# Kernel tuning notes

Hardware: AMD Instinct MI355X
Metric: run time of the kernel (lower is better)

Reference implementation:

```python
import jax, jax.numpy as jnp
import numpy as np

IGNORE_INDEX = -100
W_HARD = 0.5
W_SOFT = 0.5
TEMPERATURE = 1.0
BETA = 0.0  # forward KL branch
NORMALIZE_TOPK = True


def setup_inputs() -> dict:
    key = jax.random.key(0)
    ks = jax.random.split(key, 6)
    B, N, D, V, K = 2, 2048, 2048, 32768, 64
    student_input = jax.random.normal(ks[0], (B, N, D), dtype=jnp.float32)
    # scale weight so logits are O(1)-ish and logsumexp is well-behaved in fp32
    student_lm_head_weight = jax.random.normal(ks[1], (V, D), dtype=jnp.float32) * 0.02
    target_token_ids = jax.random.randint(ks[2], (B, N, K), 0, V, dtype=jnp.int64)
    # realistic teacher top-k logprobs: normalized over k
    target_logprobs = jax.nn.log_softmax(jax.random.normal(ks[3], (B, N, K), dtype=jnp.float32), axis=-1)
    target_mask = jax.random.randint(ks[4], (B, N, K), 0, 2, dtype=jnp.int32)
    true_labels = jax.random.randint(ks[5], (B, N), 0, V, dtype=jnp.int64)
    return {
        "student_input": student_input,
        "student_lm_head_weight": student_lm_head_weight,
        "target_token_ids": target_token_ids,
        "target_logprobs": target_logprobs,
        "target_mask": target_mask,
        "true_labels": true_labels,
    }


def reference(student_input, student_lm_head_weight, target_token_ids, target_logprobs, target_mask, true_labels):
    B, N, D = student_input.shape
    K = target_token_ids.shape[-1]
    M = B * N

    x = student_input.reshape(M, D)
    logits = x @ student_lm_head_weight.T  # (M, V)

    # ---- hard CE loss on next-token-shifted labels (sum reduction, ignore_index) ----
    labels = jnp.pad(true_labels, ((0, 0), (0, 1)), constant_values=IGNORE_INDEX)[:, 1:].reshape(M)
    lse_full = jax.nn.logsumexp(logits, axis=-1)  # (M,)
    valid = labels != IGNORE_INDEX
    safe_labels = jnp.where(valid, labels, 0)
    gold = jnp.take_along_axis(logits, safe_labels[:, None], axis=-1)[:, 0]
    ce_loss = jnp.sum(jnp.where(valid, lse_full - gold, 0.0))

    # ---- soft top-k forward-KL loss (beta == 0.0) ----
    s_logits = logits / TEMPERATURE
    s_lse = jax.nn.logsumexp(s_logits, axis=-1, keepdims=True)  # (M, 1)
    tk_ids = target_token_ids.reshape(M, K)
    s_lp_topk = jnp.take_along_axis(s_logits, tk_ids, axis=-1) - s_lse  # (M, K)
    if NORMALIZE_TOPK:
        s_lp_topk = jax.nn.log_softmax(s_lp_topk, axis=-1)
    t_lp = target_logprobs.reshape(M, K)
    mask = target_mask.reshape(M, K).astype(bool)
    fwd_kl = jnp.exp(t_lp) * (t_lp - s_lp_topk)  # per-token forward KL terms
    kd_loss = jnp.sum(jnp.where(mask, fwd_kl, 0.0))
    kd_loss = kd_loss * (TEMPERATURE ** 2)

    return W_SOFT * kd_loss + W_HARD * ce_loss
```

## Files before the change

### kernel.cpp

```cpp
#include <hip/hip_runtime.h>
#include <hip/hip_bf16.h>
#include <stdint.h>

typedef __attribute__((ext_vector_type(4))) float f32x4;
typedef __attribute__((ext_vector_type(2))) long l8x16;

#define D_DIM 2048
#define V_DIM 32768
#define M_DIM 4096
#define N_SEQ 2048
#define K_TOP 64
#define NSLOT 512
#define EBCAP 512
#define WSCALE 64.0f
#define IWSCALE 0.015625f

static __device__ __forceinline__ unsigned int f32_to_e4m3(float x) {
  float ax = fminf(fabsf(x), 448.0f);
  unsigned int s = (__float_as_uint(x) >> 31) << 7;
  if (ax >= 0.015625f) {
    unsigned int m = __float_as_uint(ax);
    unsigned int keep = m >> 20;
    unsigned int rb = (m >> 19) & 1u, st = (m & 0x7FFFFu) != 0u;
    keep += rb & (st | (keep & 1u));
    int v = (int)keep - (120 << 3);
    if (v > 0x7E) v = 0x7E;
    return s | (unsigned int)v;
  } else {
    int m = __float2int_rn(ax * 512.0f);
    return s | (unsigned int)m;
  }
}

typedef __attribute__((address_space(3))) unsigned int lds_u32_t;
typedef const __attribute__((address_space(1))) unsigned int glb_u32_t;
static __device__ __forceinline__ void gload16(const void* g, void* l) {
  __builtin_amdgcn_global_load_lds((glb_u32_t*)g, (lds_u32_t*)l, 16, 0, 0);
}

__global__ void cast_fp8_kernel(const float4* __restrict__ inA, uint2* __restrict__ outA, int nA8,
                                const float4* __restrict__ inB, uint2* __restrict__ outB, int nB8) {
  int i = blockIdx.x * blockDim.x + threadIdx.x;
  int stride = gridDim.x * blockDim.x;
  int tot = nA8 + nB8;
  for (; i < tot; i += stride) {
    const float4* in = (i < nA8) ? inA : inB;
    uint2* out = (i < nA8) ? outA : outB;
    float sc = (i < nA8) ? WSCALE : 1.0f;
    int j = (i < nA8) ? i : i - nA8;
    float4 a = in[2 * j], b = in[2 * j + 1];
    uint2 r;
    r.x = f32_to_e4m3(a.x * sc) | (f32_to_e4m3(a.y * sc) << 8) |
          (f32_to_e4m3(a.z * sc) << 16) | (f32_to_e4m3(a.w * sc) << 24);
    r.y = f32_to_e4m3(b.x * sc) | (f32_to_e4m3(b.y * sc) << 8) |
          (f32_to_e4m3(b.z * sc) << 16) | (f32_to_e4m3(b.w * sc) << 24);
    int oj = ((j >> 3) << 3) + ((j & 3) << 1) + ((j >> 2) & 1);
    out[oj] = r;
  }
}

__global__ __launch_bounds__(256) void bin_kernel(
    const int* __restrict__ tids, const int* __restrict__ tlab,
    unsigned int* __restrict__ cnt, unsigned int* __restrict__ ebuf) {
  int idx = blockIdx.x * 256 + threadIdx.x;
  if (idx >= M_DIM * (K_TOP + 1)) return;
  int m = idx / (K_TOP + 1), k = idx - m * (K_TOP + 1);
  int id;
  if (k < K_TOP) id = tids[m * K_TOP + k];
  else {
    int n = m & (N_SEQ - 1);
    if (n == N_SEQ - 1) return;
    id = tlab[m + 1];
  }
  int tile = ((m >> 8) << 7) + (id >> 8);
  unsigned int pos = atomicAdd(&cnt[tile], 1u);
  if (pos < EBCAP)
    ebuf[tile * EBCAP + pos] =
        ((unsigned int)k << 16) | ((unsigned int)(m & 255) << 8) | (unsigned int)(id & 255);
}


#define BAR do { __builtin_amdgcn_s_barrier(); asm volatile("" ::: "memory"); } while (0)
#define VMC(N) asm volatile("s_waitcnt vmcnt(" #N ")" ::: "memory")
#define PRIO1 __builtin_amdgcn_s_setprio(1)
#define PRIO0 __builtin_amdgcn_s_setprio(0)

#define LDF(BASE, R) \
  (*(const l8x16*)((BASE) + (R) * 64 + ((kqg ^ (((R) >> 1) & 3)) << 4)))
#define LDAF(BASE, MI) LDF(BASE, (MI) * 16 + fr)
#define LDBF(BASE, NI) LDF(BASE, brow + (NI) * 16 + fr)

#define STAGE(H) do { \
  int tt_ = (H) >> 2, pos_ = (H) & 3; \
  char* dst_ = ldst + ((tt_ & 1) << 15) + (pos_ << 13); \
  const unsigned char* src_ = ((pos_ & 2) ? aptr : bptr) \
      + ((pos_ & 1) ? (size_t)128 * D_DIM : (size_t)0) + (size_t)tt_ * 64; \
  gload16(src_, dst_); \
} while (0)

#define MFMA_Q(M0, U0, U1) do { \
  _Pragma("unroll") \
  for (int ni = 0; ni < 4; ++ni) \
    acc[M0][ni] = __builtin_amdgcn_mfma_f32_16x16x32_fp8_fp8((U0)[0], bF[ni][0], acc[M0][ni], 0, 0, 0); \
  _Pragma("unroll") \
  for (int ni = 0; ni < 4; ++ni) \
    acc[(M0) + 1][ni] = __builtin_amdgcn_mfma_f32_16x16x32_fp8_fp8((U1)[0], bF[ni][0], acc[(M0) + 1][ni], 0, 0, 0); \
  _Pragma("unroll") \
  for (int ni = 0; ni < 4; ++ni) \
    acc[M0][ni] = __builtin_amdgcn_mfma_f32_16x16x32_fp8_fp8((U0)[1], bF[ni][1], acc[M0][ni], 0, 0, 0); \
  _Pragma("unroll") \
  for (int ni = 0; ni < 4; ++ni) \
    acc[(M0) + 1][ni] = __builtin_amdgcn_mfma_f32_16x16x32_fp8_fp8((U1)[1], bF[ni][1], acc[(M0) + 1][ni], 0, 0, 0); \
} while (0)

#define TILE1B(T, DOST, NVM, DONEXT) do { \
  char* curA_ = ldsAroot + (((T) & 1) << 15); \
  char* nxtA_ = ldsAroot + ((((T) + 1) & 1) << 15); \
  char* nxtB_ = ldsBroot + ((((T) + 1) & 1) << 15); \
   \
  BAR; \
  if (DOST) STAGE(4 * (T) + 8); \
  PRIO1; MFMA_Q(0, a01[0], a01[1]); PRIO0; \
  a23[0] = LDAF(curA_, 2); a23[1] = LDAF(curA_, 3); \
   \
  BAR; \
  if (DOST) STAGE(4 * (T) + 9); \
  PRIO1; MFMA_Q(2, a23[0], a23[1]); PRIO0; \
  a45[0] = LDAF(curA_, 4); a45[1] = LDAF(curA_, 5); \
   \
  BAR; \
  PRIO1; MFMA_Q(4, a45[0], a45[1]); PRIO0; \
  a67[0] = LDAF(curA_, 6); a67[1] = LDAF(curA_, 7); \
  if ((NVM) == 2) { VMC(2); } else if ((NVM) == 0) { VMC(0); } \
   \
  BAR; \
  if (DOST) { STAGE(4 * (T) + 10); STAGE(4 * (T) + 11); } \
  PRIO1; MFMA_Q(6, a67[0], a67[1]); PRIO0; \
  if (DONEXT) { \
    bF[0] = LDBF(nxtB_, 0); bF[1] = LDBF(nxtB_, 1); \
    bF[2] = LDBF(nxtB_, 2); bF[3] = LDBF(nxtB_, 3); \
    a01[0] = LDAF(nxtA_, 0); a01[1] = LDAF(nxtA_, 1); \
  } \
} while (0)

__global__ __launch_bounds__(512, 2) void gemm_lse_kernel(
    const unsigned char* __restrict__ x8,
    const unsigned char* __restrict__ w8,
    float* __restrict__ pMax,
    float* __restrict__ pSum,
    const unsigned int* __restrict__ bcnt,
    const unsigned int* __restrict__ ebuf,
    float* __restrict__ gout) {
  __shared__ __align__(16) char lds[131072];

  const int bid0 = blockIdx.x;
  const int mt = (bid0 >> 4) & 15;
  const int vt = ((bid0 >> 8) << 4) | (bid0 & 15);
  const int tid = threadIdx.x, lane = tid & 63, w = tid >> 6;
  const int wr = w >> 2, wc = w & 3;
  const int fr = lane & 15, kqg = lane >> 4;
  const int brow = (wc & 1) * 64;

  const int gcol = (((tid & 3) ^ ((tid >> 3) & 3)) << 4);
  const unsigned char* aptr = x8 + (size_t)(mt * 256 + (tid >> 2)) * D_DIM + gcol;
  const unsigned char* bptr = w8 + (size_t)(vt * 256 + (tid >> 2)) * D_DIM + gcol;
  char* ldst = lds + tid * 16;

  char* ldsAroot = lds + ((2 + wr) << 13);
  char* ldsBroot = lds + ((wc >> 1) << 13);

  f32x4 acc[8][4];
#pragma unroll
  for (int i = 0; i < 8; i++)
#pragma unroll
    for (int j = 0; j < 4; j++) acc[i][j] = (f32x4){0.f, 0.f, 0.f, 0.f};

  l8x16 bF[4], a01[2], a23[2], a45[2], a67[2];

  STAGE(0); STAGE(1); STAGE(2); STAGE(3);
  STAGE(4); STAGE(5); STAGE(6); STAGE(7);
  VMC(0);
  BAR;
  bF[0] = LDBF(ldsBroot, 0); bF[1] = LDBF(ldsBroot, 1);
  bF[2] = LDBF(ldsBroot, 2); bF[3] = LDBF(ldsBroot, 3);
  a01[0] = LDAF(ldsAroot, 0); a01[1] = LDAF(ldsAroot, 1);

  for (int it = 0; it < 15; ++it) {
    TILE1B(2 * it, 1, 2, 1);
    TILE1B(2 * it + 1, 1, 2, 1);
  }
  TILE1B(30, 0, 0, 1);
  TILE1B(31, 0, 99, 0);

  const int slot = vt * 4 + wc;
#pragma unroll
  for (int mi = 0; mi < 8; mi++) {
#pragma unroll
    for (int j = 0; j < 4; j++) {
      const int row = mt * 256 + wr * 128 + mi * 16 + kqg * 4 + j;
      float v0 = acc[mi][0][j] * IWSCALE, v1 = acc[mi][1][j] * IWSCALE;
      float v2 = acc[mi][2][j] * IWSCALE, v3 = acc[mi][3][j] * IWSCALE;
      float mx = fmaxf(fmaxf(v0, v1), fmaxf(v2, v3));
      for (int s = 1; s < 16; s <<= 1) mx = fmaxf(mx, __shfl_xor(mx, s));
      float sm = __expf(v0 - mx) + __expf(v1 - mx) +
                 __expf(v2 - mx) + __expf(v3 - mx);
      for (int s = 1; s < 16; s <<= 1) sm += __shfl_xor(sm, s);
      if (fr == 0) {
        pMax[row * NSLOT + slot] = mx;
        pSum[row * NSLOT + slot] = sm;
      }
    }
  }

  const int tile = (mt << 7) + vt;
  unsigned int cn = bcnt[tile];
  if (cn > EBCAP) cn = EBCAP;
  const unsigned int* elist = ebuf + tile * EBCAP;
  float* ldsf = (float*)lds;

  __syncthreads();
#pragma unroll
  for (int half = 0; half < 2; ++half) {
    if (wr == half) {
#pragma unroll
      for (int mi = 0; mi < 8; mi++) {
        const int r0 = mi * 16 + kqg * 4;
        const int cs = (kqg & 1) << 4;
#pragma unroll
        for (int ni = 0; ni < 4; ni++) {
          const int c0 = (wc * 64 + ni * 16 + fr) ^ cs;
#pragma unroll
          for (int j = 0; j < 4; j++)
            ldsf[(r0 + j) * 256 + c0] = acc[mi][ni][j] * IWSCALE;
        }
      }
    }
    __syncthreads();
    for (unsigned int e = tid; e < cn; e += 512) {
      unsigned int u = elist[e];
      int r = (u >> 8) & 255;
      if ((r >> 7) == half) {
        int c = u & 255, k = u >> 16;
        int rl = r & 127;
        gout[(mt * 256 + r) * (K_TOP + 1) + k] = ldsf[rl * 256 + (c ^ (((rl >> 2) & 1) << 4))];
      }
    }
    __syncthreads();
  }
}

__global__ __launch_bounds__(256) void reduce_kernel(
    const float* __restrict__ pMax, const float* __restrict__ pSum,
    const float* __restrict__ gout, const float* __restrict__ t_lp,
    const int* __restrict__ t_mask, float* __restrict__ out) {
  const int tid = threadIdx.x, lane = tid & 63, w = tid >> 6;
  const int m = blockIdx.x * 4 + w;

  float msl[8], ssl[8];
  float M = -1e30f;
#pragma unroll
  for (int j = 0; j < 8; j++) {
    msl[j] = pMax[m * NSLOT + lane + j * 64];
    ssl[j] = pSum[m * NSLOT + lane + j * 64];
    M = fmaxf(M, msl[j]);
  }
  for (int s = 1; s < 64; s <<= 1) M = fmaxf(M, __shfl_xor(M, s));
  float S = 0.f;
#pragma unroll
  for (int j = 0; j < 8; j++) S += ssl[j] * __expf(msl[j] - M);
  for (int s = 1; s < 64; s <<= 1) S += __shfl_xor(S, s);
  const float lse = M + logf(S);

  const int n = m & (N_SEQ - 1);
  float ce = 0.f;
  if (n < N_SEQ - 1) ce = lse - gout[m * (K_TOP + 1) + K_TOP];

  const float g = gout[m * (K_TOP + 1) + lane];
  float gM = g;
  for (int s = 1; s < 64; s <<= 1) gM = fmaxf(gM, __shfl_xor(gM, s));
  float gE = __expf(g - gM);
  float gS = gE;
  for (int s = 1; s < 64; s <<= 1) gS += __shfl_xor(gS, s);
  const float lseK = gM + logf(gS);

  const float tl = t_lp[m * K_TOP + lane];
  const int mk = t_mask[m * K_TOP + lane];
  float kd = mk ? __expf(tl) * (tl - (g - lseK)) : 0.f;
  for (int s = 1; s < 64; s <<= 1) kd += __shfl_xor(kd, s);

  if (lane == 0) atomicAdd(out, 0.5f * kd + 0.5f * ce);
}

extern "C" void kernel_launch(void* const* d_in, const int* in_sizes, int n_in,
                              void* d_out, int out_size, void* d_ws, size_t ws_size,
                              hipStream_t stream) {
  const float* x   = (const float*)d_in[0];
  const float* Wm  = (const float*)d_in[1];
  const int* tids  = (const int*)d_in[2];
  const float* tlp = (const float*)d_in[3];
  const int* tmask = (const int*)d_in[4];
  const int* tlab  = (const int*)d_in[5];
  float* out = (float*)d_out;

  char* ws = (char*)d_ws;
  unsigned char* w8 = (unsigned char*)ws;
  unsigned char* x8 = (unsigned char*)(ws + (size_t)V_DIM * D_DIM);
  char* p = ws + (size_t)V_DIM * D_DIM + (size_t)M_DIM * D_DIM;
  float* pMax = (float*)p;                       p += (size_t)M_DIM * NSLOT * 4;
  float* pSum = (float*)p;                       p += (size_t)M_DIM * NSLOT * 4;
  float* gout = (float*)p;                       p += (size_t)M_DIM * (K_TOP + 1) * 4;
  unsigned int* bcnt = (unsigned int*)p;         p += 2048 * 4;
  unsigned int* ebuf = (unsigned int*)p;         p += (size_t)2048 * EBCAP * 4;

  hipMemsetAsync(d_out, 0, sizeof(float), stream);
  hipMemsetAsync(bcnt, 0, 2048 * 4, stream);

  bin_kernel<<<(M_DIM * (K_TOP + 1) + 255) / 256, 256, 0, stream>>>(
      tids, tlab, bcnt, ebuf);

  cast_fp8_kernel<<<8192, 256, 0, stream>>>(
      (const float4*)Wm, (uint2*)w8, (V_DIM * D_DIM) / 8,
      (const float4*)x, (uint2*)x8, (M_DIM * D_DIM) / 8);

  gemm_lse_kernel<<<(M_DIM / 256) * (V_DIM / 256), 512, 0, stream>>>(
      x8, w8, pMax, pSum, bcnt, ebuf, gout);

  reduce_kernel<<<M_DIM / 4, 256, 0, stream>>>(pMax, pSum, gout, tlp, tmask, out);
}
```

Before: 552.2 us.

## Switch GEMM mainloop to 16x16x128 scaled fp8 MFMA with 128-byte K tiles

Replaces the 16x16x32 fp8 MFMA sequence with the gfx950 scaled MFMA 16x16x128 f8f6f4 instruction, using unit scales. The K tile per stage doubles to 128 bytes, so LDS buffers, staging loads, swizzle and waitcnt counts are all resized, and the mainloop drops from 32 to 16 tiles. The cast kernel's output permutation is removed because fragments are now read as two contiguous 16-byte LDS loads. The aim is to cut MFMA instruction count and loop overhead per unit of work. It raises register and LDS pressure and changes the bank-conflict pattern.

```diff
diff --git a/kernel.cpp b/kernel.cpp
--- a/kernel.cpp
+++ b/kernel.cpp
@@ -3,7 +3,8 @@
 #include <stdint.h>
 
 typedef __attribute__((ext_vector_type(4))) float f32x4;
-typedef __attribute__((ext_vector_type(2))) long l8x16;
+typedef __attribute__((ext_vector_type(4))) int i32x4;
+typedef __attribute__((ext_vector_type(8))) int i32x8;
 
 #define D_DIM 2048
 #define V_DIM 32768
@@ -54,8 +55,7 @@
           (f32_to_e4m3(a.z * sc) << 16) | (f32_to_e4m3(a.w * sc) << 24);
     r.y = f32_to_e4m3(b.x * sc) | (f32_to_e4m3(b.y * sc) << 8) |
           (f32_to_e4m3(b.z * sc) << 16) | (f32_to_e4m3(b.w * sc) << 24);
-    int oj = ((j >> 3) << 3) + ((j & 3) << 1) + ((j >> 2) & 1);
-    out[oj] = r;
+    out[j] = r;
   }
 }
 
@@ -85,61 +85,63 @@
 #define PRIO1 __builtin_amdgcn_s_setprio(1)
 #define PRIO0 __builtin_amdgcn_s_setprio(0)
 
-#define LDF(BASE, R) \
-  (*(const l8x16*)((BASE) + (R) * 64 + ((kqg ^ (((R) >> 1) & 3)) << 4)))
-#define LDAF(BASE, MI) LDF(BASE, (MI) * 16 + fr)
-#define LDBF(BASE, NI) LDF(BASE, brow + (NI) * 16 + fr)
+#define LDQ(BASE, R, H) \
+  (*(const i32x4*)((BASE) + (R) * 128 + (((2 * kqg + (H)) ^ ((R) & 7)) << 4)))
+#define FRAG(DST, BASE, R) do { \
+  i32x4 lo_ = LDQ(BASE, R, 0), hi_ = LDQ(BASE, R, 1); \
+  DST = __builtin_shufflevector(lo_, hi_, 0, 1, 2, 3, 4, 5, 6, 7); \
+} while (0)
+#define FRAGA(DST, BASE, MI) FRAG(DST, BASE, (MI) * 16 + fr)
+#define FRAGB(DST, BASE, NI) FRAG(DST, BASE, brow + (NI) * 16 + fr)
 
 #define STAGE(H) do { \
   int tt_ = (H) >> 2, pos_ = (H) & 3; \
-  char* dst_ = ldst + ((tt_ & 1) << 15) + (pos_ << 13); \
+  char* dst_ = ldst + ((tt_ & 1) << 16) + (pos_ << 14); \
   const unsigned char* src_ = ((pos_ & 2) ? aptr : bptr) \
-      + ((pos_ & 1) ? (size_t)128 * D_DIM : (size_t)0) + (size_t)tt_ * 64; \
+      + ((pos_ & 1) ? (size_t)128 * D_DIM : (size_t)0) + (size_t)tt_ * 128; \
   gload16(src_, dst_); \
+  gload16(src_ + (size_t)64 * D_DIM, dst_ + 8192); \
 } while (0)
+
+#define MX(A_, B_, C_) __builtin_amdgcn_mfma_scale_f32_16x16x128_f8f6f4( \
+    (A_), (B_), (C_), 0, 0, 0, 0x7F7F7F7F, 0, 0x7F7F7F7F)
 
 #define MFMA_Q(M0, U0, U1) do { \
   _Pragma("unroll") \
   for (int ni = 0; ni < 4; ++ni) \
-    acc[M0][ni] = __builtin_amdgcn_mfma_f32_16x16x32_fp8_fp8((U0)[0], bF[ni][0], acc[M0][ni], 0, 0, 0); \
+    acc[M0][ni] = MX(U0, bF[ni], acc[M0][ni]); \
   _Pragma("unroll") \
   for (int ni = 0; ni < 4; ++ni) \
-    acc[(M0) + 1][ni] = __builtin_amdgcn_mfma_f32_16x16x32_fp8_fp8((U1)[0], bF[ni][0], acc[(M0) + 1][ni], 0, 0, 0); \
-  _Pragma("unroll") \
-  for (int ni = 0; ni < 4; ++ni) \
-    acc[M0][ni] = __builtin_amdgcn_mfma_f32_16x16x32_fp8_fp8((U0)[1], bF[ni][1], acc[M0][ni], 0, 0, 0); \
-  _Pragma("unroll") \
-  for (int ni = 0; ni < 4; ++ni) \
-    acc[(M0) + 1][ni] = __builtin_amdgcn_mfma_f32_16x16x32_fp8_fp8((U1)[1], bF[ni][1], acc[(M0) + 1][ni], 0, 0, 0); \
+    acc[(M0) + 1][ni] = MX(U1, bF[ni], acc[(M0) + 1][ni]); \
 } while (0)
 
 #define TILE1B(T, DOST, NVM, DONEXT) do { \
-  char* curA_ = ldsAroot + (((T) & 1) << 15); \
-  char* nxtA_ = ldsAroot + ((((T) + 1) & 1) << 15); \
-  char* nxtB_ = ldsBroot + ((((T) + 1) & 1) << 15); \
+  char* curA_ = ldsAroot + (((T) & 1) << 16); \
+  char* nxtA_ = ldsAroot + ((((T) + 1) & 1) << 16); \
+  char* nxtB_ = ldsBroot + ((((T) + 1) & 1) << 16); \
    \
   BAR; \
   if (DOST) STAGE(4 * (T) + 8); \
-  PRIO1; MFMA_Q(0, a01[0], a01[1]); PRIO0; \
-  a23[0] = LDAF(curA_, 2); a23[1] = LDAF(curA_, 3); \
+  PRIO1; MFMA_Q(0, a0, a1); PRIO0; \
+  FRAGA(a2, curA_, 2); FRAGA(a3, curA_, 3); \
    \
   BAR; \
   if (DOST) STAGE(4 * (T) + 9); \
-  PRIO1; MFMA_Q(2, a23[0], a23[1]); PRIO0; \
-  a45[0] = LDAF(curA_, 4); a45[1] = LDAF(curA_, 5); \
+  PRIO1; MFMA_Q(2, a2, a3); PRIO0; \
+  FRAGA(a0, curA_, 4); FRAGA(a1, curA_, 5); \
    \
   BAR; \
-  PRIO1; MFMA_Q(4, a45[0], a45[1]); PRIO0; \
-  a67[0] = LDAF(curA_, 6); a67[1] = LDAF(curA_, 7); \
-  if ((NVM) == 2) { VMC(2); } else if ((NVM) == 0) { VMC(0); } \
+  PRIO1; MFMA_Q(4, a0, a1); PRIO0; \
+  FRAGA(a2, curA_, 6); FRAGA(a3, curA_, 7); \
+  if ((NVM) == 4) { VMC(4); } else if ((NVM) == 0) { VMC(0); } \
    \
   BAR; \
   if (DOST) { STAGE(4 * (T) + 10); STAGE(4 * (T) + 11); } \
-  PRIO1; MFMA_Q(6, a67[0], a67[1]); PRIO0; \
+  PRIO1; MFMA_Q(6, a2, a3); PRIO0; \
   if (DONEXT) { \
-    bF[0] = LDBF(nxtB_, 0); bF[1] = LDBF(nxtB_, 1); \
-    bF[2] = LDBF(nxtB_, 2); bF[3] = LDBF(nxtB_, 3); \
-    a01[0] = LDAF(nxtA_, 0); a01[1] = LDAF(nxtA_, 1); \
+    FRAGB(bF[0], nxtB_, 0); FRAGB(bF[1], nxtB_, 1); \
+    FRAGB(bF[2], nxtB_, 2); FRAGB(bF[3], nxtB_, 3); \
+    FRAGA(a0, nxtA_, 0); FRAGA(a1, nxtA_, 1); \
   } \
 } while (0)
 
@@ -161,13 +163,13 @@
   const int fr = lane & 15, kqg = lane >> 4;
   const int brow = (wc & 1) * 64;
 
-  const int gcol = (((tid & 3) ^ ((tid >> 3) & 3)) << 4);
-  const unsigned char* aptr = x8 + (size_t)(mt * 256 + (tid >> 2)) * D_DIM + gcol;
-  const unsigned char* bptr = w8 + (size_t)(vt * 256 + (tid >> 2)) * D_DIM + gcol;
+  const int gcol = (((tid & 7) ^ ((tid >> 3) & 7)) << 4);
+  const unsigned char* aptr = x8 + (size_t)(mt * 256 + (tid >> 3)) * D_DIM + gcol;
+  const unsigned char* bptr = w8 + (size_t)(vt * 256 + (tid >> 3)) * D_DIM + gcol;
   char* ldst = lds + tid * 16;
 
-  char* ldsAroot = lds + ((2 + wr) << 13);
-  char* ldsBroot = lds + ((wc >> 1) << 13);
+  char* ldsAroot = lds + ((2 + wr) << 14);
+  char* ldsBroot = lds + ((wc >> 1) << 14);
 
   f32x4 acc[8][4];
 #pragma unroll
@@ -175,22 +177,22 @@
 #pragma unroll
     for (int j = 0; j < 4; j++) acc[i][j] = (f32x4){0.f, 0.f, 0.f, 0.f};
 
-  l8x16 bF[4], a01[2], a23[2], a45[2], a67[2];
+  i32x8 bF[4], a0, a1, a2, a3;
 
   STAGE(0); STAGE(1); STAGE(2); STAGE(3);
   STAGE(4); STAGE(5); STAGE(6); STAGE(7);
   VMC(0);
   BAR;
-  bF[0] = LDBF(ldsBroot, 0); bF[1] = LDBF(ldsBroot, 1);
-  bF[2] = LDBF(ldsBroot, 2); bF[3] = LDBF(ldsBroot, 3);
-  a01[0] = LDAF(ldsAroot, 0); a01[1] = LDAF(ldsAroot, 1);
-
-  for (int it = 0; it < 15; ++it) {
-    TILE1B(2 * it, 1, 2, 1);
-    TILE1B(2 * it + 1, 1, 2, 1);
-  }
-  TILE1B(30, 0, 0, 1);
-  TILE1B(31, 0, 99, 0);
+  FRAGB(bF[0], ldsBroot, 0); FRAGB(bF[1], ldsBroot, 1);
+  FRAGB(bF[2], ldsBroot, 2); FRAGB(bF[3], ldsBroot, 3);
+  FRAGA(a0, ldsAroot, 0); FRAGA(a1, ldsAroot, 1);
+
+  for (int it = 0; it < 7; ++it) {
+    TILE1B(2 * it, 1, 4, 1);
+    TILE1B(2 * it + 1, 1, 4, 1);
+  }
+  TILE1B(14, 0, 0, 1);
+  TILE1B(15, 0, 99, 0);
 
   const int slot = vt * 4 + wc;
 #pragma unroll
```

New measurement: 635.8 us. +15.1%, slower.

## Shrink GEMM block tile to 128x256 with 256 threads and smaller LDS

Applied to the files above, without the earlier changes.

Changes the fused FP8 GEMM+LSE kernel from 256x256 tiles with 8 waves to 128x256 tiles with 4 waves. LDS drops from 128KB to 48KB with a reorganized double-buffered staging layout, and the gather epilogue now runs in four passes. The bin kernel's tiling and entry-buffer capacity are adjusted to match. The aim is more concurrent blocks and better occupancy and latency hiding, at the cost of less B-operand reuse per block. It also doubles the grid size and the number of bucket counters.

```diff
diff --git a/kernel.cpp b/kernel.cpp
--- a/kernel.cpp
+++ b/kernel.cpp
@@ -11,7 +11,7 @@
 #define N_SEQ 2048
 #define K_TOP 64
 #define NSLOT 512
-#define EBCAP 512
+#define EBCAP 256
 #define WSCALE 64.0f
 #define IWSCALE 0.015625f
 
@@ -72,11 +72,11 @@
     if (n == N_SEQ - 1) return;
     id = tlab[m + 1];
   }
-  int tile = ((m >> 8) << 7) + (id >> 8);
+  int tile = ((m >> 7) << 7) + (id >> 8);
   unsigned int pos = atomicAdd(&cnt[tile], 1u);
   if (pos < EBCAP)
     ebuf[tile * EBCAP + pos] =
-        ((unsigned int)k << 16) | ((unsigned int)(m & 255) << 8) | (unsigned int)(id & 255);
+        ((unsigned int)k << 16) | ((unsigned int)(m & 127) << 8) | (unsigned int)(id & 255);
 }
 
 
@@ -90,12 +90,12 @@
 #define LDAF(BASE, MI) LDF(BASE, (MI) * 16 + fr)
 #define LDBF(BASE, NI) LDF(BASE, brow + (NI) * 16 + fr)
 
-#define STAGE(H) do { \
-  int tt_ = (H) >> 2, pos_ = (H) & 3; \
-  char* dst_ = ldst + ((tt_ & 1) << 15) + (pos_ << 13); \
-  const unsigned char* src_ = ((pos_ & 2) ? aptr : bptr) \
-      + ((pos_ & 1) ? (size_t)128 * D_DIM : (size_t)0) + (size_t)tt_ * 64; \
+#define STAGE(TT, POS) do { \
+  char* dst_ = ldst + (((TT) & 1) ? 24576 : 0) + ((POS) << 13); \
+  const unsigned char* src_ = (((POS) == 2) ? aptr : bptr) \
+      + (((POS) == 1) ? (size_t)128 * D_DIM : (size_t)0) + (size_t)(TT) * 64; \
   gload16(src_, dst_); \
+  gload16(src_ + (size_t)64 * D_DIM, dst_ + 4096); \
 } while (0)
 
 #define MFMA_Q(M0, U0, U1) do { \
@@ -114,27 +114,29 @@
 } while (0)
 
 #define TILE1B(T, DOST, NVM, DONEXT) do { \
-  char* curA_ = ldsAroot + (((T) & 1) << 15); \
-  char* nxtA_ = ldsAroot + ((((T) + 1) & 1) << 15); \
-  char* nxtB_ = ldsBroot + ((((T) + 1) & 1) << 15); \
+  char* base_ = lds + (((T) & 1) ? 24576 : 0); \
+  char* nbase_ = lds + ((((T) + 1) & 1) ? 24576 : 0); \
+  char* curA_ = base_ + 16384; \
+  char* nxtA_ = nbase_ + 16384; \
+  char* nxtB_ = nbase_ + bOff; \
    \
   BAR; \
-  if (DOST) STAGE(4 * (T) + 8); \
+  if (DOST) STAGE((T) + 2, 0); \
   PRIO1; MFMA_Q(0, a01[0], a01[1]); PRIO0; \
   a23[0] = LDAF(curA_, 2); a23[1] = LDAF(curA_, 3); \
    \
   BAR; \
-  if (DOST) STAGE(4 * (T) + 9); \
+  if (DOST) STAGE((T) + 2, 1); \
   PRIO1; MFMA_Q(2, a23[0], a23[1]); PRIO0; \
   a45[0] = LDAF(curA_, 4); a45[1] = LDAF(curA_, 5); \
    \
   BAR; \
   PRIO1; MFMA_Q(4, a45[0], a45[1]); PRIO0; \
   a67[0] = LDAF(curA_, 6); a67[1] = LDAF(curA_, 7); \
-  if ((NVM) == 2) { VMC(2); } else if ((NVM) == 0) { VMC(0); } \
+  if ((NVM) == 4) { VMC(4); } else if ((NVM) == 0) { VMC(0); } \
    \
   BAR; \
-  if (DOST) { STAGE(4 * (T) + 10); STAGE(4 * (T) + 11); } \
+  if (DOST) STAGE((T) + 2, 2); \
   PRIO1; MFMA_Q(6, a67[0], a67[1]); PRIO0; \
   if (DONEXT) { \
     bF[0] = LDBF(nxtB_, 0); bF[1] = LDBF(nxtB_, 1); \
@@ -143,7 +145,7 @@
   } \
 } while (0)
 
-__global__ __launch_bounds__(512, 2) void gemm_lse_kernel(
+__global__ __launch_bounds__(256, 2) void gemm_lse_kernel(
     const unsigned char* __restrict__ x8,
     const unsigned char* __restrict__ w8,
     float* __restrict__ pMax,
@@ -151,24 +153,21 @@
     const unsigned int* __restrict__ bcnt,
     const unsigned int* __restrict__ ebuf,
     float* __restrict__ gout) {
-  __shared__ __align__(16) char lds[131072];
+  __shared__ __align__(16) char lds[49152];
 
   const int bid0 = blockIdx.x;
-  const int mt = (bid0 >> 4) & 15;
-  const int vt = ((bid0 >> 8) << 4) | (bid0 & 15);
+  const int mt = (bid0 >> 4) & 31;
+  const int vt = ((bid0 >> 9) << 4) | (bid0 & 15);
   const int tid = threadIdx.x, lane = tid & 63, w = tid >> 6;
-  const int wr = w >> 2, wc = w & 3;
   const int fr = lane & 15, kqg = lane >> 4;
-  const int brow = (wc & 1) * 64;
+  const int brow = (w & 1) * 64;
+  const int bOff = (w >> 1) << 13;
 
   const int gcol = (((tid & 3) ^ ((tid >> 3) & 3)) << 4);
-  const unsigned char* aptr = x8 + (size_t)(mt * 256 + (tid >> 2)) * D_DIM + gcol;
+  const unsigned char* aptr = x8 + (size_t)(mt * 128 + (tid >> 2)) * D_DIM + gcol;
   const unsigned char* bptr = w8 + (size_t)(vt * 256 + (tid >> 2)) * D_DIM + gcol;
   char* ldst = lds + tid * 16;
 
-  char* ldsAroot = lds + ((2 + wr) << 13);
-  char* ldsBroot = lds + ((wc >> 1) << 13);
-
   f32x4 acc[8][4];
 #pragma unroll
   for (int i = 0; i < 8; i++)
@@ -177,27 +176,31 @@
 
   l8x16 bF[4], a01[2], a23[2], a45[2], a67[2];
 
-  STAGE(0); STAGE(1); STAGE(2); STAGE(3);
-  STAGE(4); STAGE(5); STAGE(6); STAGE(7);
+  STAGE(0, 0); STAGE(0, 1); STAGE(0, 2);
+  STAGE(1, 0); STAGE(1, 1); STAGE(1, 2);
   VMC(0);
   BAR;
-  bF[0] = LDBF(ldsBroot, 0); bF[1] = LDBF(ldsBroot, 1);
-  bF[2] = LDBF(ldsBroot, 2); bF[3] = LDBF(ldsBroot, 3);
-  a01[0] = LDAF(ldsAroot, 0); a01[1] = LDAF(ldsAroot, 1);
+  {
+    char* b0_ = lds + bOff;
+    char* a0_ = lds + 16384;
+    bF[0] = LDBF(b0_, 0); bF[1] = LDBF(b0_, 1);
+    bF[2] = LDBF(b0_, 2); bF[3] = LDBF(b0_, 3);
+    a01[0] = LDAF(a0_, 0); a01[1] = LDAF(a0_, 1);
+  }
 
   for (int it = 0; it < 15; ++it) {
-    TILE1B(2 * it, 1, 2, 1);
-    TILE1B(2 * it + 1, 1, 2, 1);
+    TILE1B(2 * it, 1, 4, 1);
+    TILE1B(2 * it + 1, 1, 4, 1);
   }
   TILE1B(30, 0, 0, 1);
   TILE1B(31, 0, 99, 0);
 
-  const int slot = vt * 4 + wc;
+  const int slot = vt * 4 + w;
 #pragma unroll
   for (int mi = 0; mi < 8; mi++) {
 #pragma unroll
     for (int j = 0; j < 4; j++) {
-      const int row = mt * 256 + wr * 128 + mi * 16 + kqg * 4 + j;
+      const int row = mt * 128 + mi * 16 + kqg * 4 + j;
       float v0 = acc[mi][0][j] * IWSCALE, v1 = acc[mi][1][j] * IWSCALE;
       float v2 = acc[mi][2][j] * IWSCALE, v3 = acc[mi][3][j] * IWSCALE;
       float mx = fmaxf(fmaxf(v0, v1), fmaxf(v2, v3));
@@ -220,29 +223,28 @@
 
   __syncthreads();
 #pragma unroll
-  for (int half = 0; half < 2; ++half) {
-    if (wr == half) {
-#pragma unroll
-      for (int mi = 0; mi < 8; mi++) {
-        const int r0 = mi * 16 + kqg * 4;
-        const int cs = (kqg & 1) << 4;
-#pragma unroll
-        for (int ni = 0; ni < 4; ni++) {
-          const int c0 = (wc * 64 + ni * 16 + fr) ^ cs;
-#pragma unroll
-          for (int j = 0; j < 4; j++)
-            ldsf[(r0 + j) * 256 + c0] = acc[mi][ni][j] * IWSCALE;
-        }
+  for (int pass = 0; pass < 4; ++pass) {
+#pragma unroll
+    for (int mm = 0; mm < 2; ++mm) {
+      const int mi = 2 * pass + mm;
+      const int r0 = mm * 16 + kqg * 4;
+      const int cs = (kqg & 1) << 4;
+#pragma unroll
+      for (int ni = 0; ni < 4; ni++) {
+        const int c0 = (w * 64 + ni * 16 + fr) ^ cs;
+#pragma unroll
+        for (int j = 0; j < 4; j++)
+          ldsf[(r0 + j) * 256 + c0] = acc[mi][ni][j] * IWSCALE;
       }
     }
     __syncthreads();
-    for (unsigned int e = tid; e < cn; e += 512) {
+    for (unsigned int e = tid; e < cn; e += 256) {
       unsigned int u = elist[e];
       int r = (u >> 8) & 255;
-      if ((r >> 7) == half) {
+      if ((r >> 5) == pass) {
         int c = u & 255, k = u >> 16;
-        int rl = r & 127;
-        gout[(mt * 256 + r) * (K_TOP + 1) + k] = ldsf[rl * 256 + (c ^ (((rl >> 2) & 1) << 4))];
+        int rl = r & 31;
+        gout[(mt * 128 + r) * (K_TOP + 1) + k] = ldsf[rl * 256 + (c ^ (((rl >> 2) & 1) << 4))];
       }
     }
     __syncthreads();
@@ -309,11 +311,11 @@
   float* pMax = (float*)p;                       p += (size_t)M_DIM * NSLOT * 4;
   float* pSum = (float*)p;                       p += (size_t)M_DIM * NSLOT * 4;
   float* gout = (float*)p;                       p += (size_t)M_DIM * (K_TOP + 1) * 4;
-  unsigned int* bcnt = (unsigned int*)p;         p += 2048 * 4;
-  unsigned int* ebuf = (unsigned int*)p;         p += (size_t)2048 * EBCAP * 4;
+  unsigned int* bcnt = (unsigned int*)p;         p += 4096 * 4;
+  unsigned int* ebuf = (unsigned int*)p;         p += (size_t)4096 * EBCAP * 4;
 
   hipMemsetAsync(d_out, 0, sizeof(float), stream);
-  hipMemsetAsync(bcnt, 0, 2048 * 4, stream);
+  hipMemsetAsync(bcnt, 0, 4096 * 4, stream);
 
   bin_kernel<<<(M_DIM * (K_TOP + 1) + 255) / 256, 256, 0, stream>>>(
       tids, tlab, bcnt, ebuf);
@@ -322,7 +324,7 @@
       (const float4*)Wm, (uint2*)w8, (V_DIM * D_DIM) / 8,
       (const float4*)x, (uint2*)x8, (M_DIM * D_DIM) / 8);
 
-  gemm_lse_kernel<<<(M_DIM / 256) * (V_DIM / 256), 512, 0, stream>>>(
+  gemm_lse_kernel<<<(M_DIM / 128) * (V_DIM / 256), 256, 0, stream>>>(
       x8, w8, pMax, pSum, bcnt, ebuf, gout);
 
   reduce_kernel<<<M_DIM / 4, 256, 0, stream>>>(pMax, pSum, gout, tlp, tmask, out);
```

New measurement: 503.2 us. 8.9% less time.
